# Kernel tuning notes

Hardware: AMD Instinct MI355X
Metric: run time of the kernel (lower is better)

Reference implementation:

```python
import jax, jax.numpy as jnp
import numpy as np

ALPHA = 0.2  # LeakyReLU negative slope
NEG_INF = -9e15


def setup_inputs() -> dict:
    key = jax.random.key(0)
    ks = jax.random.split(key, 6)
    B, N, F_IN, F_OUT = 4, 1024, 64, 64
    h = jax.random.normal(ks[0], (B, N, F_IN), dtype=jnp.float32)
    adj = jax.random.randint(ks[1], (B, N, N), 0, 2, dtype=jnp.int32)
    lin_w = jax.random.normal(ks[2], (F_OUT, F_IN), dtype=jnp.float32) * (1.0 / np.sqrt(F_IN))
    lin_b = jax.random.normal(ks[3], (F_OUT,), dtype=jnp.float32) * 0.02
    W_w = jax.random.normal(ks[4], (F_OUT, 2 * F_OUT), dtype=jnp.float32) * (1.0 / np.sqrt(2 * F_OUT))
    a = jax.random.normal(ks[5], (F_OUT, 1), dtype=jnp.float32) * (1.414 / np.sqrt(F_OUT))
    return {"h": h, "adj": adj, "lin_w": lin_w, "lin_b": lin_b, "W_w": W_w, "a": a}


def reference(h, adj, lin_w, lin_b, W_w, a):
    F_OUT = lin_w.shape[0]
    # h' = Linear(h): (B, N, F_OUT)
    hp = jnp.einsum('bni,oi->bno', h, lin_w) + lin_b
    # W @ concat(h_i, h_j) == h_i @ W1^T + h_j @ W2^T  (same math, no 2F concat)
    W1, W2 = W_w[:, :F_OUT], W_w[:, F_OUT:]
    u = jnp.einsum('bnf,of->bno', hp, W1)  # source/row term   (B, N, F_OUT)
    v = jnp.einsum('bnf,of->bno', hp, W2)  # target/col term   (B, N, F_OUT)
    s = u[:, :, None, :] + v[:, None, :, :]        # (B, N, N, F_OUT)
    s = jnp.where(s > 0, s, ALPHA * s)             # LeakyReLU
    e = jnp.einsum('bijf,f->bij', s, a[:, 0])      # (B, N, N)
    e = jnp.where(adj > 0, e, NEG_INF)
    attention = jax.nn.softmax(e, axis=2)
    h_prime = jnp.einsum('bij,bjf->bif', attention, hp)
    return jax.nn.elu(h_prime)
```

## Files before the change

kernel.cpp:

```cpp
#include <hip/hip_runtime.h>
#include <hip/hip_bf16.h>
#include <math.h>

constexpr int B = 4;
constexpr int N = 1024;
constexpr float NEGINF = -9000000000000000.0f;

__global__ __launch_bounds__(256) void gat_prep(
    const float* __restrict__ h, const float* __restrict__ lin_w,
    const float* __restrict__ lin_b, const float* __restrict__ W_w,
    const float* __restrict__ a_g,
    float* __restrict__ hp, float* __restrict__ u_out, float* __restrict__ vT,
    float* __restrict__ au_out, float* __restrict__ av_out) {
  __shared__ float hs[64 * 18];
  __shared__ float wl[64 * 68];
  __shared__ float w1[64 * 68];
  __shared__ float w2[64 * 68];
  __shared__ float hpT[64 * 18];
  __shared__ float vt_s[64 * 17];
  __shared__ float ared[2][16 * 17];
  __shared__ float lb_s[64], a_s[64];

  const int b = blockIdx.x >> 6;
  const int n0 = (blockIdx.x & 63) << 4;
  const int tid = threadIdx.x;

  if (tid < 64) { lb_s[tid] = lin_b[tid]; a_s[tid] = a_g[tid]; }
  for (int idx = tid; idx < 1024; idx += 256) {
    const int r = idx >> 6, c = idx & 63;
    hs[c * 18 + r] = h[((b << 10) + n0 + r) * 64 + c];
  }
  for (int idx = tid; idx < 4096; idx += 256) {
    const int o = idx >> 6, f = idx & 63;
    wl[f * 68 + o] = lin_w[idx];
    w1[f * 68 + o] = W_w[o * 128 + f];
    w2[f * 68 + o] = W_w[o * 128 + 64 + f];
  }
  __syncthreads();

  const int tf = tid & 15, tn = tid >> 4;
  float ahp[4];
#pragma unroll
  for (int r = 0; r < 4; ++r) ahp[r] = lb_s[tf * 4 + r];
#pragma unroll 8
  for (int k = 0; k < 64; ++k) {
    const float hv = hs[k * 18 + tn];
    const float4 l4 = *(const float4*)&wl[k * 68 + tf * 4];
    ahp[0] = fmaf(hv, l4.x, ahp[0]);
    ahp[1] = fmaf(hv, l4.y, ahp[1]);
    ahp[2] = fmaf(hv, l4.z, ahp[2]);
    ahp[3] = fmaf(hv, l4.w, ahp[3]);
  }
  const int row = (b << 10) + n0 + tn;
  *(float4*)&hp[row * 64 + tf * 4] = make_float4(ahp[0], ahp[1], ahp[2], ahp[3]);
#pragma unroll
  for (int r = 0; r < 4; ++r) hpT[(tf * 4 + r) * 18 + tn] = ahp[r];
  __syncthreads();

  float aU[4] = {0.f, 0.f, 0.f, 0.f}, aV[4] = {0.f, 0.f, 0.f, 0.f};
#pragma unroll 8
  for (int k = 0; k < 64; ++k) {
    const float hv = hpT[k * 18 + tn];
    const float4 u4 = *(const float4*)&w1[k * 68 + tf * 4];
    const float4 v4 = *(const float4*)&w2[k * 68 + tf * 4];
    aU[0] = fmaf(hv, u4.x, aU[0]);
    aU[1] = fmaf(hv, u4.y, aU[1]);
    aU[2] = fmaf(hv, u4.z, aU[2]);
    aU[3] = fmaf(hv, u4.w, aU[3]);
    aV[0] = fmaf(hv, v4.x, aV[0]);
    aV[1] = fmaf(hv, v4.y, aV[1]);
    aV[2] = fmaf(hv, v4.z, aV[2]);
    aV[3] = fmaf(hv, v4.w, aV[3]);
  }
  *(float4*)&u_out[row * 64 + tf * 4] = make_float4(aU[0], aU[1], aU[2], aU[3]);
  float aup = 0.f, avp = 0.f;
#pragma unroll
  for (int r = 0; r < 4; ++r) {
    vt_s[(tf * 4 + r) * 17 + tn] = aV[r];
    aup = fmaf(a_s[tf * 4 + r], aU[r], aup);
    avp = fmaf(a_s[tf * 4 + r], aV[r], avp);
  }
  ared[0][tn * 17 + tf] = aup;
  ared[1][tn * 17 + tf] = avp;
  __syncthreads();
  for (int idx = tid; idx < 1024; idx += 256) {
    const int f = idx >> 4, n = idx & 15;
    vT[(((b << 6) + f) << 10) + n0 + n] = vt_s[f * 17 + n];
  }
  if (tid < 32) {
    const int which = tid >> 4, rr = tid & 15;
    float s2 = 0.f;
#pragma unroll
    for (int t = 0; t < 16; ++t) s2 += ared[which][rr * 17 + t];
    if (which == 0) au_out[(b << 10) + n0 + rr] = s2;
    else av_out[(b << 10) + n0 + rr] = s2;
  }
}

__global__ __launch_bounds__(256) void gat_attn(
    const float* __restrict__ u_g, const float* __restrict__ vT,
    const float* __restrict__ hp, const int* __restrict__ adj,
    const float* __restrict__ a_g, const float* __restrict__ au_g,
    const float* __restrict__ av_g, float* __restrict__ out) {
  __shared__ float p_s[4 * 1024];
  __shared__ float u_s[64 * 4];
  __shared__ float a_s[64];
  __shared__ float au_s[4];
  __shared__ float wred[4][4];
  __shared__ float wsum[4][4];
  __shared__ float rinv_s[4];

  const int b = blockIdx.x >> 8;
  const int i0 = (blockIdx.x & 255) << 2;
  const int tid = threadIdx.x;
  const int lane = tid & 63, w = tid >> 6;
  const int j0 = tid << 2;

  if (tid < 64) a_s[tid] = a_g[tid];
  if (tid < 4) au_s[tid] = au_g[(b << 10) + i0 + tid];
  {
    const int i = tid >> 6, f = tid & 63;
    u_s[f * 4 + i] = u_g[((b << 10) + i0 + i) * 64 + f];
  }
  __syncthreads();

  float e[4][4];
#pragma unroll
  for (int i = 0; i < 4; ++i)
#pragma unroll
    for (int k = 0; k < 4; ++k) e[i][k] = 0.f;

  const float* vb = vT + ((b << 6) << 10) + j0;
#pragma unroll 4
  for (int f = 0; f < 64; ++f) {
    const float af = a_s[f];
    const float4 v4 = *(const float4*)&vb[f << 10];
    const float4 u4 = *(const float4*)&u_s[f * 4];
    const float uu[4] = {u4.x, u4.y, u4.z, u4.w};
    const float vv[4] = {v4.x, v4.y, v4.z, v4.w};
#pragma unroll
    for (int i = 0; i < 4; ++i)
#pragma unroll
      for (int k = 0; k < 4; ++k)
        e[i][k] = fmaf(af, fabsf(uu[i] + vv[k]), e[i][k]);
  }
  const float4 av4 = *(const float4*)&av_g[(b << 10) + j0];
  const float avv[4] = {0.6f * av4.x, 0.6f * av4.y, 0.6f * av4.z, 0.6f * av4.w};
  float au6[4];
#pragma unroll
  for (int i = 0; i < 4; ++i) au6[i] = 0.6f * au_s[i];
  const int* adjb = adj + (((b << 10) + i0) << 10) + j0;
#pragma unroll
  for (int i = 0; i < 4; ++i) {
    const int4 ad = *(const int4*)&adjb[i << 10];
    const int adv[4] = {ad.x, ad.y, ad.z, ad.w};
#pragma unroll
    for (int k = 0; k < 4; ++k) {
      const float ev = fmaf(0.4f, e[i][k], au6[i] + avv[k]);
      e[i][k] = adv[k] > 0 ? ev : NEGINF;
    }
  }

#pragma unroll
  for (int i = 0; i < 4; ++i) {
    float mm = fmaxf(fmaxf(e[i][0], e[i][1]), fmaxf(e[i][2], e[i][3]));
#pragma unroll
    for (int off = 32; off; off >>= 1) mm = fmaxf(mm, __shfl_xor(mm, off));
    if (lane == 0) wred[w][i] = mm;
  }
  __syncthreads();
#pragma unroll
  for (int i = 0; i < 4; ++i) {
    const float mi = fmaxf(fmaxf(wred[0][i], wred[1][i]),
                           fmaxf(wred[2][i], wred[3][i]));
#pragma unroll
    for (int k = 0; k < 4; ++k) e[i][k] = __expf(e[i][k] - mi);
    float ss = e[i][0] + e[i][1] + e[i][2] + e[i][3];
#pragma unroll
    for (int off = 32; off; off >>= 1) ss += __shfl_xor(ss, off);
    if (lane == 0) wsum[w][i] = ss;
  }
  __syncthreads();
  if (tid < 4)
    rinv_s[tid] = 1.0f / (wsum[0][tid] + wsum[1][tid] + wsum[2][tid] + wsum[3][tid]);

#pragma unroll
  for (int k = 0; k < 4; ++k)
    *(float4*)&p_s[(tid << 2) + (k << 10)] =
        make_float4(e[0][k], e[1][k], e[2][k], e[3][k]);
  __syncthreads();

  const int fq = tid & 15, g = tid >> 4;
  float4 acc[4];
#pragma unroll
  for (int i = 0; i < 4; ++i) acc[i] = make_float4(0.f, 0.f, 0.f, 0.f);
  const float* hpb = hp + (b << 16) + (fq << 2);
#pragma unroll 4
  for (int jj = 0; jj < 64; ++jj) {
    const int j = (g << 6) + jj;
    const float4 h4 = *(const float4*)&hpb[j << 6];
    const float4 p4 = *(const float4*)&p_s[(j & ~3) + ((j & 3) << 10)];
    acc[0].x = fmaf(p4.x, h4.x, acc[0].x);
    acc[0].y = fmaf(p4.x, h4.y, acc[0].y);
    acc[0].z = fmaf(p4.x, h4.z, acc[0].z);
    acc[0].w = fmaf(p4.x, h4.w, acc[0].w);
    acc[1].x = fmaf(p4.y, h4.x, acc[1].x);
    acc[1].y = fmaf(p4.y, h4.y, acc[1].y);
    acc[1].z = fmaf(p4.y, h4.z, acc[1].z);
    acc[1].w = fmaf(p4.y, h4.w, acc[1].w);
    acc[2].x = fmaf(p4.z, h4.x, acc[2].x);
    acc[2].y = fmaf(p4.z, h4.y, acc[2].y);
    acc[2].z = fmaf(p4.z, h4.z, acc[2].z);
    acc[2].w = fmaf(p4.z, h4.w, acc[2].w);
    acc[3].x = fmaf(p4.w, h4.x, acc[3].x);
    acc[3].y = fmaf(p4.w, h4.y, acc[3].y);
    acc[3].z = fmaf(p4.w, h4.z, acc[3].z);
    acc[3].w = fmaf(p4.w, h4.w, acc[3].w);
  }
  __syncthreads();
#pragma unroll
  for (int i = 0; i < 4; ++i)
    *(float4*)&p_s[(g << 8) + (i << 6) + (fq << 2)] = acc[i];
  __syncthreads();
  {
    const int i = tid >> 6, f = tid & 63;
    float r = 0.f;
#pragma unroll
    for (int gg = 0; gg < 16; ++gg) r += p_s[(gg << 8) + (i << 6) + f];
    r *= rinv_s[i];
    out[((b << 10) + i0 + i) * 64 + f] = r > 0.f ? r : expm1f(r);
  }
}

extern "C" void kernel_launch(void* const* d_in, const int* in_sizes, int n_in,
                              void* d_out, int out_size, void* d_ws, size_t ws_size,
                              hipStream_t stream) {
  const float* h = (const float*)d_in[0];
  const int* adj = (const int*)d_in[1];
  const float* lin_w = (const float*)d_in[2];
  const float* lin_b = (const float*)d_in[3];
  const float* W_w = (const float*)d_in[4];
  const float* a = (const float*)d_in[5];
  float* outp = (float*)d_out;

  float* ws = (float*)d_ws;
  float* hp = ws;
  float* u = ws + 262144;
  float* vT = ws + 524288;
  float* au = ws + 786432;
  float* av = ws + 790528;

  gat_prep<<<dim3(256), dim3(256), 0, stream>>>(h, lin_w, lin_b, W_w, a,
                                                hp, u, vT, au, av);
  gat_attn<<<dim3(1024), dim3(256), 0, stream>>>(u, vT, hp, adj, a, au, av, outp);
}
```

Measured before the change: 111.5 us.

## Process eight query rows per 512-thread block with shuffle-based aggregation reduction

The attention kernel now handles 8 rows per block with 512 threads, each thread owning 2 columns across 8 rows instead of 4x4, which halves the number of blocks. The aim is to amortise the hp and vT reads over more rows and cut redundant global traffic. The aggregation stage interleaves j across groups, reduces partial sums with wavefront shuffles, and then does a smaller cross-wave shared-memory reduction. In exchange, registers per thread and shared memory per block both grow, and with only 512 blocks there may be fewer blocks per CU to hide latency.

Measured after the change: 112.8 us. Within noise of the previous version (+1.2%).

```diff
diff --git a/kernel.cpp b/kernel.cpp
--- a/kernel.cpp
+++ b/kernel.cpp
@@ -97,136 +97,168 @@
   }
 }
 
-__global__ __launch_bounds__(256) void gat_attn(
+__global__ __launch_bounds__(512) void gat_attn(
     const float* __restrict__ u_g, const float* __restrict__ vT,
     const float* __restrict__ hp, const int* __restrict__ adj,
     const float* __restrict__ a_g, const float* __restrict__ au_g,
     const float* __restrict__ av_g, float* __restrict__ out) {
-  __shared__ float p_s[4 * 1024];
-  __shared__ float u_s[64 * 4];
+  __shared__ float p_s[8 * 1024];
+  __shared__ float wp_s[8 * 512];
+  __shared__ float u_s[64 * 8];
   __shared__ float a_s[64];
-  __shared__ float au_s[4];
-  __shared__ float wred[4][4];
-  __shared__ float wsum[4][4];
-  __shared__ float rinv_s[4];
-
-  const int b = blockIdx.x >> 8;
-  const int i0 = (blockIdx.x & 255) << 2;
+  __shared__ float au_s[8];
+  __shared__ float wred[8][8];
+  __shared__ float wsum[8][8];
+  __shared__ float rinv_s[8];
+
+  const int b = blockIdx.x >> 7;
+  const int i0 = (blockIdx.x & 127) << 3;
   const int tid = threadIdx.x;
   const int lane = tid & 63, w = tid >> 6;
-  const int j0 = tid << 2;
+  const int j0 = tid << 1;
 
   if (tid < 64) a_s[tid] = a_g[tid];
-  if (tid < 4) au_s[tid] = au_g[(b << 10) + i0 + tid];
+  if (tid < 8) au_s[tid] = au_g[(b << 10) + i0 + tid];
   {
     const int i = tid >> 6, f = tid & 63;
-    u_s[f * 4 + i] = u_g[((b << 10) + i0 + i) * 64 + f];
-  }
-  __syncthreads();
-
-  float e[4][4];
-#pragma unroll
-  for (int i = 0; i < 4; ++i)
-#pragma unroll
-    for (int k = 0; k < 4; ++k) e[i][k] = 0.f;
+    u_s[f * 8 + i] = u_g[((b << 10) + i0 + i) * 64 + f];
+  }
+  __syncthreads();
+
+  float e[8][2];
+#pragma unroll
+  for (int i = 0; i < 8; ++i) { e[i][0] = 0.f; e[i][1] = 0.f; }
 
   const float* vb = vT + ((b << 6) << 10) + j0;
 #pragma unroll 4
   for (int f = 0; f < 64; ++f) {
     const float af = a_s[f];
-    const float4 v4 = *(const float4*)&vb[f << 10];
-    const float4 u4 = *(const float4*)&u_s[f * 4];
-    const float uu[4] = {u4.x, u4.y, u4.z, u4.w};
-    const float vv[4] = {v4.x, v4.y, v4.z, v4.w};
-#pragma unroll
-    for (int i = 0; i < 4; ++i)
-#pragma unroll
-      for (int k = 0; k < 4; ++k)
-        e[i][k] = fmaf(af, fabsf(uu[i] + vv[k]), e[i][k]);
-  }
-  const float4 av4 = *(const float4*)&av_g[(b << 10) + j0];
-  const float avv[4] = {0.6f * av4.x, 0.6f * av4.y, 0.6f * av4.z, 0.6f * av4.w};
-  float au6[4];
-#pragma unroll
-  for (int i = 0; i < 4; ++i) au6[i] = 0.6f * au_s[i];
+    const float2 v2 = *(const float2*)&vb[f << 10];
+    const float4 ua = *(const float4*)&u_s[f * 8];
+    const float4 ub = *(const float4*)&u_s[f * 8 + 4];
+    const float uu[8] = {ua.x, ua.y, ua.z, ua.w, ub.x, ub.y, ub.z, ub.w};
+    const float vv[2] = {v2.x, v2.y};
+#pragma unroll
+    for (int i = 0; i < 8; ++i) {
+      e[i][0] = fmaf(af, fabsf(uu[i] + vv[0]), e[i][0]);
+      e[i][1] = fmaf(af, fabsf(uu[i] + vv[1]), e[i][1]);
+    }
+  }
+  const float2 av2 = *(const float2*)&av_g[(b << 10) + j0];
+  const float avv[2] = {0.6f * av2.x, 0.6f * av2.y};
+  float au6[8];
+#pragma unroll
+  for (int i = 0; i < 8; ++i) au6[i] = 0.6f * au_s[i];
   const int* adjb = adj + (((b << 10) + i0) << 10) + j0;
 #pragma unroll
-  for (int i = 0; i < 4; ++i) {
-    const int4 ad = *(const int4*)&adjb[i << 10];
-    const int adv[4] = {ad.x, ad.y, ad.z, ad.w};
-#pragma unroll
-    for (int k = 0; k < 4; ++k) {
-      const float ev = fmaf(0.4f, e[i][k], au6[i] + avv[k]);
-      e[i][k] = adv[k] > 0 ? ev : NEGINF;
-    }
-  }
-
-#pragma unroll
-  for (int i = 0; i < 4; ++i) {
-    float mm = fmaxf(fmaxf(e[i][0], e[i][1]), fmaxf(e[i][2], e[i][3]));
+  for (int i = 0; i < 8; ++i) {
+    const int2 ad = *(const int2*)&adjb[i << 10];
+    const float e0 = fmaf(0.4f, e[i][0], au6[i] + avv[0]);
+    const float e1 = fmaf(0.4f, e[i][1], au6[i] + avv[1]);
+    e[i][0] = ad.x > 0 ? e0 : NEGINF;
+    e[i][1] = ad.y > 0 ? e1 : NEGINF;
+  }
+
+#pragma unroll
+  for (int i = 0; i < 8; ++i) {
+    float mm = fmaxf(e[i][0], e[i][1]);
 #pragma unroll
     for (int off = 32; off; off >>= 1) mm = fmaxf(mm, __shfl_xor(mm, off));
     if (lane == 0) wred[w][i] = mm;
   }
   __syncthreads();
 #pragma unroll
-  for (int i = 0; i < 4; ++i) {
-    const float mi = fmaxf(fmaxf(wred[0][i], wred[1][i]),
-                           fmaxf(wred[2][i], wred[3][i]));
-#pragma unroll
-    for (int k = 0; k < 4; ++k) e[i][k] = __expf(e[i][k] - mi);
-    float ss = e[i][0] + e[i][1] + e[i][2] + e[i][3];
+  for (int i = 0; i < 8; ++i) {
+    float mi = wred[0][i];
+#pragma unroll
+    for (int ww = 1; ww < 8; ++ww) mi = fmaxf(mi, wred[ww][i]);
+    e[i][0] = __expf(e[i][0] - mi);
+    e[i][1] = __expf(e[i][1] - mi);
+    float ss = e[i][0] + e[i][1];
 #pragma unroll
     for (int off = 32; off; off >>= 1) ss += __shfl_xor(ss, off);
     if (lane == 0) wsum[w][i] = ss;
   }
   __syncthreads();
-  if (tid < 4)
-    rinv_s[tid] = 1.0f / (wsum[0][tid] + wsum[1][tid] + wsum[2][tid] + wsum[3][tid]);
-
-#pragma unroll
-  for (int k = 0; k < 4; ++k)
-    *(float4*)&p_s[(tid << 2) + (k << 10)] =
-        make_float4(e[0][k], e[1][k], e[2][k], e[3][k]);
+  if (tid < 8) {
+    float st = 0.f;
+#pragma unroll
+    for (int ww = 0; ww < 8; ++ww) st += wsum[ww][tid];
+    rinv_s[tid] = 1.0f / st;
+  }
+#pragma unroll
+  for (int k = 0; k < 2; ++k) {
+    const int j = j0 + k;
+    *(float4*)&p_s[j << 3] = make_float4(e[0][k], e[1][k], e[2][k], e[3][k]);
+    *(float4*)&p_s[(j << 3) + 4] = make_float4(e[4][k], e[5][k], e[6][k], e[7][k]);
+  }
   __syncthreads();
 
   const int fq = tid & 15, g = tid >> 4;
-  float4 acc[4];
-#pragma unroll
-  for (int i = 0; i < 4; ++i) acc[i] = make_float4(0.f, 0.f, 0.f, 0.f);
+  float4 acc[8];
+#pragma unroll
+  for (int i = 0; i < 8; ++i) acc[i] = make_float4(0.f, 0.f, 0.f, 0.f);
   const float* hpb = hp + (b << 16) + (fq << 2);
 #pragma unroll 4
-  for (int jj = 0; jj < 64; ++jj) {
-    const int j = (g << 6) + jj;
+  for (int jj = 0; jj < 32; ++jj) {
+    const int j = (jj << 5) + g;
     const float4 h4 = *(const float4*)&hpb[j << 6];
-    const float4 p4 = *(const float4*)&p_s[(j & ~3) + ((j & 3) << 10)];
-    acc[0].x = fmaf(p4.x, h4.x, acc[0].x);
-    acc[0].y = fmaf(p4.x, h4.y, acc[0].y);
-    acc[0].z = fmaf(p4.x, h4.z, acc[0].z);
-    acc[0].w = fmaf(p4.x, h4.w, acc[0].w);
-    acc[1].x = fmaf(p4.y, h4.x, acc[1].x);
-    acc[1].y = fmaf(p4.y, h4.y, acc[1].y);
-    acc[1].z = fmaf(p4.y, h4.z, acc[1].z);
-    acc[1].w = fmaf(p4.y, h4.w, acc[1].w);
-    acc[2].x = fmaf(p4.z, h4.x, acc[2].x);
-    acc[2].y = fmaf(p4.z, h4.y, acc[2].y);
-    acc[2].z = fmaf(p4.z, h4.z, acc[2].z);
-    acc[2].w = fmaf(p4.z, h4.w, acc[2].w);
-    acc[3].x = fmaf(p4.w, h4.x, acc[3].x);
-    acc[3].y = fmaf(p4.w, h4.y, acc[3].y);
-    acc[3].z = fmaf(p4.w, h4.z, acc[3].z);
-    acc[3].w = fmaf(p4.w, h4.w, acc[3].w);
-  }
-  __syncthreads();
-#pragma unroll
-  for (int i = 0; i < 4; ++i)
-    *(float4*)&p_s[(g << 8) + (i << 6) + (fq << 2)] = acc[i];
+    const float4 pA = *(const float4*)&p_s[j << 3];
+    const float4 pB = *(const float4*)&p_s[(j << 3) + 4];
+    acc[0].x = fmaf(pA.x, h4.x, acc[0].x);
+    acc[0].y = fmaf(pA.x, h4.y, acc[0].y);
+    acc[0].z = fmaf(pA.x, h4.z, acc[0].z);
+    acc[0].w = fmaf(pA.x, h4.w, acc[0].w);
+    acc[1].x = fmaf(pA.y, h4.x, acc[1].x);
+    acc[1].y = fmaf(pA.y, h4.y, acc[1].y);
+    acc[1].z = fmaf(pA.y, h4.z, acc[1].z);
+    acc[1].w = fmaf(pA.y, h4.w, acc[1].w);
+    acc[2].x = fmaf(pA.z, h4.x, acc[2].x);
+    acc[2].y = fmaf(pA.z, h4.y, acc[2].y);
+    acc[2].z = fmaf(pA.z, h4.z, acc[2].z);
+    acc[2].w = fmaf(pA.z, h4.w, acc[2].w);
+    acc[3].x = fmaf(pA.w, h4.x, acc[3].x);
+    acc[3].y = fmaf(pA.w, h4.y, acc[3].y);
+    acc[3].z = fmaf(pA.w, h4.z, acc[3].z);
+    acc[3].w = fmaf(pA.w, h4.w, acc[3].w);
+    acc[4].x = fmaf(pB.x, h4.x, acc[4].x);
+    acc[4].y = fmaf(pB.x, h4.y, acc[4].y);
+    acc[4].z = fmaf(pB.x, h4.z, acc[4].z);
+    acc[4].w = fmaf(pB.x, h4.w, acc[4].w);
+    acc[5].x = fmaf(pB.y, h4.x, acc[5].x);
+    acc[5].y = fmaf(pB.y, h4.y, acc[5].y);
+    acc[5].z = fmaf(pB.y, h4.z, acc[5].z);
+    acc[5].w = fmaf(pB.y, h4.w, acc[5].w);
+    acc[6].x = fmaf(pB.z, h4.x, acc[6].x);
+    acc[6].y = fmaf(pB.z, h4.y, acc[6].y);
+    acc[6].z = fmaf(pB.z, h4.z, acc[6].z);
+    acc[6].w = fmaf(pB.z, h4.w, acc[6].w);
+    acc[7].x = fmaf(pB.w, h4.x, acc[7].x);
+    acc[7].y = fmaf(pB.w, h4.y, acc[7].y);
+    acc[7].z = fmaf(pB.w, h4.z, acc[7].z);
+    acc[7].w = fmaf(pB.w, h4.w, acc[7].w);
+  }
+#pragma unroll
+  for (int i = 0; i < 8; ++i) {
+#pragma unroll
+    for (int off = 16; off <= 32; off <<= 1) {
+      acc[i].x += __shfl_xor(acc[i].x, off);
+      acc[i].y += __shfl_xor(acc[i].y, off);
+      acc[i].z += __shfl_xor(acc[i].z, off);
+      acc[i].w += __shfl_xor(acc[i].w, off);
+    }
+  }
+  if (lane < 16) {
+#pragma unroll
+    for (int i = 0; i < 8; ++i)
+      *(float4*)&wp_s[((w << 3) + i) << 6 | (fq << 2)] = acc[i];
+  }
   __syncthreads();
   {
     const int i = tid >> 6, f = tid & 63;
     float r = 0.f;
 #pragma unroll
-    for (int gg = 0; gg < 16; ++gg) r += p_s[(gg << 8) + (i << 6) + f];
+    for (int ww = 0; ww < 8; ++ww) r += wp_s[((ww << 3) + i) << 6 | f];
     r *= rinv_s[i];
     out[((b << 10) + i0 + i) * 64 + f] = r > 0.f ? r : expm1f(r);
   }
@@ -252,5 +284,5 @@
 
   gat_prep<<<dim3(256), dim3(256), 0, stream>>>(h, lin_w, lin_b, W_w, a,
                                                 hp, u, vT, au, av);
-  gat_attn<<<dim3(1024), dim3(256), 0, stream>>>(u, vT, hp, adj, a, au, av, outp);
+  gat_attn<<<dim3(512), dim3(512), 0, stream>>>(u, vT, hp, adj, a, au, av, outp);
 }
```

## Restructure prep kernel to one output per thread with more, smaller blocks

Applied to the files above, without the earlier changes.

The projection kernel now launches 512 blocks of 512 threads, each block covering 8 rows, and each thread computes a single output feature instead of a 4-wide register tile. The per-row reductions for au and av move from a shared-memory table to wavefront shuffles. The aim is more parallelism across the GPU and fewer shared-memory stages in the small prep kernel. In exchange, each block reloads and transposes all three weight matrices for only 8 rows, which doubles the total weight staging traffic, and the per-thread FMA loops lose register-level reuse.

New measurement: 110.3 us. No clear change (-1.0%).

```diff
diff --git a/kernel.cpp b/kernel.cpp
--- a/kernel.cpp
+++ b/kernel.cpp
@@ -6,94 +6,68 @@
 constexpr int N = 1024;
 constexpr float NEGINF = -9000000000000000.0f;
 
-__global__ __launch_bounds__(256) void gat_prep(
+__global__ __launch_bounds__(512) void gat_prep(
     const float* __restrict__ h, const float* __restrict__ lin_w,
     const float* __restrict__ lin_b, const float* __restrict__ W_w,
     const float* __restrict__ a_g,
-    float* __restrict__ hp, float* __restrict__ u_out, float* __restrict__ vT,
+    float* __restrict__ hp_g, float* __restrict__ u_out, float* __restrict__ vT_g,
     float* __restrict__ au_out, float* __restrict__ av_out) {
-  __shared__ float hs[64 * 18];
-  __shared__ float wl[64 * 68];
-  __shared__ float w1[64 * 68];
-  __shared__ float w2[64 * 68];
-  __shared__ float hpT[64 * 18];
-  __shared__ float vt_s[64 * 17];
-  __shared__ float ared[2][16 * 17];
-  __shared__ float lb_s[64], a_s[64];
-
-  const int b = blockIdx.x >> 6;
-  const int n0 = (blockIdx.x & 63) << 4;
+  __shared__ float wlT[64 * 65];
+  __shared__ float w1T[64 * 65];
+  __shared__ float w2T[64 * 65];
+  __shared__ float hs[512];
+  __shared__ float hp_s[512];
+  __shared__ float v_s[64 * 9];
+  __shared__ float a_s[64];
+
+  const int b = blockIdx.x >> 7;
+  const int n0 = (blockIdx.x & 127) << 3;
   const int tid = threadIdx.x;
-
-  if (tid < 64) { lb_s[tid] = lin_b[tid]; a_s[tid] = a_g[tid]; }
-  for (int idx = tid; idx < 1024; idx += 256) {
-    const int r = idx >> 6, c = idx & 63;
-    hs[c * 18 + r] = h[((b << 10) + n0 + r) * 64 + c];
-  }
-  for (int idx = tid; idx < 4096; idx += 256) {
-    const int o = idx >> 6, f = idx & 63;
-    wl[f * 68 + o] = lin_w[idx];
-    w1[f * 68 + o] = W_w[o * 128 + f];
-    w2[f * 68 + o] = W_w[o * 128 + 64 + f];
-  }
-  __syncthreads();
-
-  const int tf = tid & 15, tn = tid >> 4;
-  float ahp[4];
-#pragma unroll
-  for (int r = 0; r < 4; ++r) ahp[r] = lb_s[tf * 4 + r];
+  const int lane = tid & 63, w = tid >> 6;
+  const int tn = w, tf = lane;
+
+  if (tid < 64) a_s[tid] = a_g[tid];
+  for (int idx = tid; idx < 4096; idx += 512) {
+    const int o = idx >> 6, k = idx & 63;
+    wlT[k * 65 + o] = lin_w[idx];
+    w1T[k * 65 + o] = W_w[o * 128 + k];
+    w2T[k * 65 + o] = W_w[o * 128 + 64 + k];
+  }
+  hs[tid] = h[(((b << 10) + n0) << 6) + tid];
+  __syncthreads();
+
+  float hpv = lin_b[tf];
+#pragma unroll 8
+  for (int k = 0; k < 64; ++k)
+    hpv = fmaf(hs[tn * 64 + k], wlT[k * 65 + tf], hpv);
+  const int row = (b << 10) + n0 + tn;
+  hp_g[(row << 6) + tf] = hpv;
+  hp_s[tn * 64 + tf] = hpv;
+  __syncthreads();
+
+  float uu = 0.f, vv = 0.f;
 #pragma unroll 8
   for (int k = 0; k < 64; ++k) {
-    const float hv = hs[k * 18 + tn];
-    const float4 l4 = *(const float4*)&wl[k * 68 + tf * 4];
-    ahp[0] = fmaf(hv, l4.x, ahp[0]);
-    ahp[1] = fmaf(hv, l4.y, ahp[1]);
-    ahp[2] = fmaf(hv, l4.z, ahp[2]);
-    ahp[3] = fmaf(hv, l4.w, ahp[3]);
-  }
-  const int row = (b << 10) + n0 + tn;
-  *(float4*)&hp[row * 64 + tf * 4] = make_float4(ahp[0], ahp[1], ahp[2], ahp[3]);
-#pragma unroll
-  for (int r = 0; r < 4; ++r) hpT[(tf * 4 + r) * 18 + tn] = ahp[r];
-  __syncthreads();
-
-  float aU[4] = {0.f, 0.f, 0.f, 0.f}, aV[4] = {0.f, 0.f, 0.f, 0.f};
-#pragma unroll 8
-  for (int k = 0; k < 64; ++k) {
-    const float hv = hpT[k * 18 + tn];
-    const float4 u4 = *(const float4*)&w1[k * 68 + tf * 4];
-    const float4 v4 = *(const float4*)&w2[k * 68 + tf * 4];
-    aU[0] = fmaf(hv, u4.x, aU[0]);
-    aU[1] = fmaf(hv, u4.y, aU[1]);
-    aU[2] = fmaf(hv, u4.z, aU[2]);
-    aU[3] = fmaf(hv, u4.w, aU[3]);
-    aV[0] = fmaf(hv, v4.x, aV[0]);
-    aV[1] = fmaf(hv, v4.y, aV[1]);
-    aV[2] = fmaf(hv, v4.z, aV[2]);
-    aV[3] = fmaf(hv, v4.w, aV[3]);
-  }
-  *(float4*)&u_out[row * 64 + tf * 4] = make_float4(aU[0], aU[1], aU[2], aU[3]);
-  float aup = 0.f, avp = 0.f;
-#pragma unroll
-  for (int r = 0; r < 4; ++r) {
-    vt_s[(tf * 4 + r) * 17 + tn] = aV[r];
-    aup = fmaf(a_s[tf * 4 + r], aU[r], aup);
-    avp = fmaf(a_s[tf * 4 + r], aV[r], avp);
-  }
-  ared[0][tn * 17 + tf] = aup;
-  ared[1][tn * 17 + tf] = avp;
-  __syncthreads();
-  for (int idx = tid; idx < 1024; idx += 256) {
-    const int f = idx >> 4, n = idx & 15;
-    vT[(((b << 6) + f) << 10) + n0 + n] = vt_s[f * 17 + n];
-  }
-  if (tid < 32) {
-    const int which = tid >> 4, rr = tid & 15;
-    float s2 = 0.f;
-#pragma unroll
-    for (int t = 0; t < 16; ++t) s2 += ared[which][rr * 17 + t];
-    if (which == 0) au_out[(b << 10) + n0 + rr] = s2;
-    else av_out[(b << 10) + n0 + rr] = s2;
+    const float hh = hp_s[tn * 64 + k];
+    uu = fmaf(hh, w1T[k * 65 + tf], uu);
+    vv = fmaf(hh, w2T[k * 65 + tf], vv);
+  }
+  u_out[(row << 6) + tf] = uu;
+  v_s[tf * 9 + tn] = vv;
+  float aup = a_s[tf] * uu, avp = a_s[tf] * vv;
+#pragma unroll
+  for (int off = 32; off; off >>= 1) {
+    aup += __shfl_xor(aup, off);
+    avp += __shfl_xor(avp, off);
+  }
+  if (tf == 0) {
+    au_out[row] = aup;
+    av_out[row] = avp;
+  }
+  __syncthreads();
+  {
+    const int f = tid >> 3, n = tid & 7;
+    vT_g[(((b << 6) + f) << 10) + n0 + n] = v_s[f * 9 + n];
   }
 }
 
@@ -250,7 +224,7 @@
   float* au = ws + 786432;
   float* av = ws + 790528;
 
-  gat_prep<<<dim3(256), dim3(256), 0, stream>>>(h, lin_w, lin_b, W_w, a,
+  gat_prep<<<dim3(512), dim3(512), 0, stream>>>(h, lin_w, lin_b, W_w, a,
                                                 hp, u, vT, au, av);
   gat_attn<<<dim3(1024), dim3(256), 0, stream>>>(u, vT, hp, adj, a, au, av, outp);
 }
```
